# Performance work log

Measured on AMD Instinct MI355X. Metric: run time of the kernel, lower is better.

Reference implementation:

```python
import jax, jax.numpy as jnp
import numpy as np

N_HEAD = 16
N_EMBD = 2048


def _rope(x):
    # x: (B, H, L, D). FAITHFUL to source: _apply_rope unpacks (B, L, H, D) on a
    # (B, H, L, D) tensor, so rotation angle = head_index * inv_freq, broadcast over
    # all sequence positions (a latent bug in the original, reproduced exactly).
    B, H, L, D = x.shape
    inv_freq = 1.0 / (10000.0 ** (jnp.arange(0, D, 2, dtype=jnp.float32) / D))  # (D/2,)
    theta = jnp.arange(H, dtype=jnp.float32)[:, None] * inv_freq[None, :]       # (H, D/2)
    cos = jnp.cos(theta)[None, :, None, :]  # (1, H, 1, D/2)
    sin = jnp.sin(theta)[None, :, None, :]
    xp = x.astype(jnp.float32).reshape(B, H, L, D // 2, 2)
    x0, x1 = xp[..., 0], xp[..., 1]
    r0 = x0 * cos - x1 * sin
    r1 = x0 * sin + x1 * cos
    return jnp.stack([r0, r1], axis=-1).reshape(B, H, L, D).astype(x.dtype)


def setup_inputs() -> dict:
    key = jax.random.key(0)
    k1, k2, k3 = jax.random.split(key, 3)
    B, L, C = 2, 2048, N_EMBD
    s = 1.0 / np.sqrt(C).astype(np.float32)
    x = jax.random.normal(k1, (B, L, C), dtype=jnp.float32)
    w_attn = jax.random.normal(k2, (3 * C, C), dtype=jnp.float32) * s
    w_proj = jax.random.normal(k3, (C, C), dtype=jnp.float32) * s
    return {"x": x, "w_attn": w_attn, "w_proj": w_proj}


def reference(x, w_attn, w_proj):
    B, L, C = x.shape
    H = N_HEAD
    D = C // H
    qkv = x @ w_attn.T                       # (B, L, 3C)
    q, k, v = jnp.split(qkv, 3, axis=2)
    q = q.reshape(B, L, H, D).transpose(0, 2, 1, 3)  # (B, H, L, D)
    k = k.reshape(B, L, H, D).transpose(0, 2, 1, 3)
    v = v.reshape(B, L, H, D).transpose(0, 2, 1, 3)
    q = _rope(q)
    k = _rope(k)
    attn = jnp.einsum('bhqd,bhkd->bhqk', q, k) * (1.0 / np.sqrt(D).astype(np.float32))
    causal = jnp.tril(jnp.ones((L, L), dtype=bool))
    attn = jnp.where(causal[None, None], attn, -jnp.inf)
    attn = jax.nn.softmax(attn, axis=-1)
    y = jnp.einsum('bhqk,bhkd->bhqd', attn, v)
    y = y.transpose(0, 2, 1, 3).reshape(B, L, C)
    return y @ w_proj.T
```

## Files before the change

### kernel.cpp

```cpp
#include <hip/hip_runtime.h>

typedef __attribute__((ext_vector_type(8))) short bf16x8;
typedef __attribute__((ext_vector_type(4))) float f32x4;

__device__ __forceinline__ unsigned short f2bf(float f) {
  unsigned int u = __float_as_uint(f);
  u += 0x7FFF + ((u >> 16) & 1);
  return (unsigned short)(u >> 16);
}

__device__ __forceinline__ void gload_lds16(const void* g, void* l) {
  __builtin_amdgcn_global_load_lds(
      (const __attribute__((address_space(1))) unsigned int*)g,
      (__attribute__((address_space(3))) unsigned int*)l,
      16, 0, 0);
}

__global__ void cast_f32_to_bf16(const float* __restrict__ in,
                                 unsigned short* __restrict__ out, int n4) {
  int stride = gridDim.x * blockDim.x;
  for (int i = blockIdx.x * blockDim.x + threadIdx.x; i < n4; i += stride) {
    float4 v = ((const float4*)in)[i];
    ushort4 o;
    o.x = f2bf(v.x); o.y = f2bf(v.y); o.z = f2bf(v.z); o.w = f2bf(v.w);
    ((ushort4*)out)[i] = o;
  }
}

template<int EPI>
__global__ __launch_bounds__(256, 2)
void gemm_bt(const unsigned short* __restrict__ A,
             const unsigned short* __restrict__ Bw,
             float* __restrict__ Cf,
             unsigned short* __restrict__ Qo,
             unsigned short* __restrict__ Ko,
             unsigned short* __restrict__ Vo,
             int M, int N, int K, int Lseq) {
  __shared__ unsigned short As[128 * 32];
  __shared__ unsigned short Bs[128 * 32];
  const int tid = threadIdx.x;
  const int lane = tid & 63, w = tid >> 6;
  const int wm = w >> 1, wn = w & 1;
  const int g4 = lane >> 4, r16 = lane & 15;
  const long arow0 = (long)blockIdx.y * 128;
  const long brow0 = (long)blockIdx.x * 128;

  f32x4 acc[4][4];
#pragma unroll
  for (int i = 0; i < 4; ++i)
#pragma unroll
    for (int j = 0; j < 4; ++j) acc[i][j] = (f32x4){0.f, 0.f, 0.f, 0.f};

  for (int k0 = 0; k0 < K; k0 += 32) {
#pragma unroll
    for (int c = 0; c < 2; ++c) {
      int off = (w << 11) + (c << 10) + (lane << 4);
      int row = off >> 6;
      int cole = (off & 63) >> 1;
      gload_lds16(A + (arow0 + row) * (long)K + k0 + cole,
                  (char*)As + (w << 11) + (c << 10));
      gload_lds16(Bw + (brow0 + row) * (long)K + k0 + cole,
                  (char*)Bs + (w << 11) + (c << 10));
    }
    __syncthreads();
    bf16x8 af[4], bf[4];
#pragma unroll
    for (int mf = 0; mf < 4; ++mf)
      af[mf] = *(const bf16x8*)((const char*)As +
                                ((64 * wm + 16 * mf + r16) << 6) + (g4 << 4));
#pragma unroll
    for (int nf = 0; nf < 4; ++nf)
      bf[nf] = *(const bf16x8*)((const char*)Bs +
                                ((64 * wn + 16 * nf + r16) << 6) + (g4 << 4));
#pragma unroll
    for (int mf = 0; mf < 4; ++mf)
#pragma unroll
      for (int nf = 0; nf < 4; ++nf)
        acc[mf][nf] = __builtin_amdgcn_mfma_f32_16x16x32_bf16(
            af[mf], bf[nf], acc[mf][nf], 0, 0, 0);
    __syncthreads();
  }

  const float qscale = 0.08838834764831845f;
#pragma unroll
  for (int mf = 0; mf < 4; ++mf) {
#pragma unroll
    for (int nf = 0; nf < 4; ++nf) {
#pragma unroll
      for (int i = 0; i < 4; ++i) {
        long row = arow0 + 64 * wm + 16 * mf + 4 * g4 + i;
        long col = brow0 + 64 * wn + 16 * nf + r16;
        float v = acc[mf][nf][i];
        if (EPI == 0) {
          Cf[row * N + col] = v;
        } else {
          int which = (int)(col >> 11);
          int h = ((int)col >> 7) & 15;
          int d = (int)col & 127;
          int b = (int)(row >> 11);
          int l = (int)row & 2047;
          long bhead = (long)(b * 16 + h);
          if (which == 0)
            Qo[(bhead * Lseq + l) * 128 + d] = f2bf(v * qscale);
          else if (which == 1)
            Ko[(bhead * Lseq + l) * 128 + d] = f2bf(v);
          else
            Vo[(bhead * 128 + d) * Lseq + l] = f2bf(v);
        }
      }
    }
  }
}

__global__ __launch_bounds__(256, 2)
void attn_fwd(const unsigned short* __restrict__ Q,
              const unsigned short* __restrict__ K,
              const unsigned short* __restrict__ Vt,
              unsigned short* __restrict__ Y, int L) {
  const int D = 128;
  const int id = blockIdx.x;
  const int g = id & 7, kk = id >> 3;
  const int bh = (g << 2) + (kk >> 5);
  const int qt = 31 - (kk & 31);
  const int tid = threadIdx.x, lane = tid & 63, w = tid >> 6;
  const int g4 = lane >> 4, r16 = lane & 15;
  const int q0 = qt * 64;

  __shared__ unsigned short Klds[2 * 64 * 128];
  __shared__ unsigned short Vlds[2 * 128 * 64];
  __shared__ unsigned short P[4][16][72];

  const unsigned short* Qh = Q + (long)bh * L * D;
  const unsigned short* Kh = K + (long)bh * L * D;
  const unsigned short* Vh = Vt + (long)bh * D * L;

#define STAGE_TILE(kt_, buf_)                                                 \
  do {                                                                        \
    const int kbase_ = (kt_) * 64;                                            \
    _Pragma("unroll")                                                         \
    for (int r_ = 0; r_ < 4; ++r_) {                                          \
      int off_ = (tid << 4) + (r_ << 12);                                     \
      int krow_ = off_ >> 8, kcb_ = (off_ >> 4) & 15;                         \
      int kcbs_ = kcb_ ^ (krow_ & 7);                                         \
      gload_lds16(Kh + (long)(kbase_ + krow_) * 128 + kcbs_ * 8,              \
                  (char*)Klds + (buf_)*16384 + (w << 10) + (r_ << 12));       \
      int vrow_ = off_ >> 7, vcb_ = (off_ >> 4) & 7;                          \
      int vcbs_ = vcb_ ^ (vrow_ & 7);                                         \
      gload_lds16(Vh + (long)vrow_ * L + kbase_ + vcbs_ * 8,                  \
                  (char*)Vlds + (buf_)*16384 + (w << 10) + (r_ << 12));       \
    }                                                                         \
  } while (0)

  bf16x8 qf[4];
  {
    long qrow = q0 + 16 * w + r16;
#pragma unroll
    for (int ks = 0; ks < 4; ++ks)
      qf[ks] = *(const bf16x8*)(Qh + qrow * D + ks * 32 + g4 * 8);
  }
  f32x4 o[8];
#pragma unroll
  for (int j = 0; j < 8; ++j) o[j] = (f32x4){0.f, 0.f, 0.f, 0.f};
  float mrun[4] = {-1e30f, -1e30f, -1e30f, -1e30f};
  float lrun[4] = {0.f, 0.f, 0.f, 0.f};

  int cur = 0;
  STAGE_TILE(0, 0);

  for (int kt = 0; kt <= qt; ++kt) {
    if (kt < qt) {
      STAGE_TILE(kt + 1, cur ^ 1);
      asm volatile("s_waitcnt vmcnt(8)" ::: "memory");
    } else {
      asm volatile("s_waitcnt vmcnt(0)" ::: "memory");
    }
    __builtin_amdgcn_s_barrier();

    const char* Kl = (const char*)Klds + cur * 16384;
    const char* Vl = (const char*)Vlds + cur * 16384;

    f32x4 s[4];
#pragma unroll
    for (int nf = 0; nf < 4; ++nf) s[nf] = (f32x4){0.f, 0.f, 0.f, 0.f};
#pragma unroll
    for (int ks = 0; ks < 4; ++ks) {
#pragma unroll
      for (int nf = 0; nf < 4; ++nf) {
        int row = 16 * nf + r16;
        bf16x8 kf = *(const bf16x8*)(Kl + row * 256 +
                                     (((ks * 4 + g4) ^ (row & 7)) << 4));
        s[nf] = __builtin_amdgcn_mfma_f32_16x16x32_bf16(qf[ks], kf, s[nf], 0, 0, 0);
      }
    }

    const bool diag = (kt == qt);
#pragma unroll
    for (int i = 0; i < 4; ++i) {
      int qg = q0 + 16 * w + 4 * g4 + i;
      float sv[4];
      float rmax = -1e30f;
#pragma unroll
      for (int nf = 0; nf < 4; ++nf) {
        float t = s[nf][i];
        if (diag && (kt * 64 + 16 * nf + r16) > qg) t = -1e30f;
        sv[nf] = t;
        rmax = fmaxf(rmax, t);
      }
      rmax = fmaxf(rmax, __shfl_xor(rmax, 1));
      rmax = fmaxf(rmax, __shfl_xor(rmax, 2));
      rmax = fmaxf(rmax, __shfl_xor(rmax, 4));
      rmax = fmaxf(rmax, __shfl_xor(rmax, 8));
      float mnew = fmaxf(mrun[i], rmax);
      float corr = __expf(mrun[i] - mnew);
      mrun[i] = mnew;
      float rs = 0.f;
#pragma unroll
      for (int nf = 0; nf < 4; ++nf) {
        float pv = __expf(sv[nf] - mnew);
        P[w][4 * g4 + i][16 * nf + r16] = f2bf(pv);
        rs += pv;
      }
      rs += __shfl_xor(rs, 1);
      rs += __shfl_xor(rs, 2);
      rs += __shfl_xor(rs, 4);
      rs += __shfl_xor(rs, 8);
      lrun[i] = lrun[i] * corr + rs;
#pragma unroll
      for (int nf2 = 0; nf2 < 8; ++nf2) o[nf2][i] *= corr;
    }
#pragma unroll
    for (int ks2 = 0; ks2 < 2; ++ks2) {
      bf16x8 pf = *(const bf16x8*)(&P[w][r16][ks2 * 32 + g4 * 8]);
#pragma unroll
      for (int nf2 = 0; nf2 < 8; ++nf2) {
        int row = 16 * nf2 + r16;
        bf16x8 vf = *(const bf16x8*)(Vl + row * 128 +
                                     (((ks2 * 4 + g4) ^ (row & 7)) << 4));
        o[nf2] = __builtin_amdgcn_mfma_f32_16x16x32_bf16(pf, vf, o[nf2], 0, 0, 0);
      }
    }
    asm volatile("" ::: "memory");
    __builtin_amdgcn_s_barrier();
    cur ^= 1;
  }
#undef STAGE_TILE

  const int b = bh >> 4, h = bh & 15;
#pragma unroll
  for (int nf2 = 0; nf2 < 8; ++nf2) {
#pragma unroll
    for (int i = 0; i < 4; ++i) {
      long row = (long)b * L + q0 + 16 * w + 4 * g4 + i;
      float v = o[nf2][i] / lrun[i];
      Y[row * 2048 + h * 128 + 16 * nf2 + r16] = f2bf(v);
    }
  }
}

extern "C" void kernel_launch(void* const* d_in, const int* in_sizes, int n_in,
                              void* d_out, int out_size, void* d_ws,
                              size_t ws_size, hipStream_t stream) {
  const float* x = (const float*)d_in[0];
  const float* wa = (const float*)d_in[1];
  const float* wp = (const float*)d_in[2];
  float* out = (float*)d_out;
  const int B = 2, L = 2048, C = 2048;
  const int M = B * L;

  unsigned short* xb = (unsigned short*)d_ws;
  unsigned short* wab = xb + (size_t)M * C;
  unsigned short* wpb = wab + (size_t)3 * C * C;
  unsigned short* Qb = wpb + (size_t)C * C;
  unsigned short* Kb = Qb + (size_t)M * C;
  unsigned short* Vb = Kb + (size_t)M * C;
  unsigned short* Yb = Vb + (size_t)M * C;

  cast_f32_to_bf16<<<2048, 256, 0, stream>>>(x, xb, M * C / 4);
  cast_f32_to_bf16<<<2048, 256, 0, stream>>>(wa, wab, 3 * C * C / 4);
  cast_f32_to_bf16<<<1024, 256, 0, stream>>>(wp, wpb, C * C / 4);

  gemm_bt<1><<<dim3(3 * C / 128, M / 128), 256, 0, stream>>>(
      xb, wab, nullptr, Qb, Kb, Vb, M, 3 * C, C, L);

  attn_fwd<<<1024, 256, 0, stream>>>(Qb, Kb, Vb, Yb, L);

  gemm_bt<0><<<dim3(C / 128, M / 128), 256, 0, stream>>>(
      Yb, wpb, out, nullptr, nullptr, nullptr, M, C, C, L);
}
```

Before: 343.7 us.

## Double-buffer GEMM LDS tiles with swizzle, XCD-aware block remap, higher occupancy

The GEMM kernel now double-buffers its A/B LDS tiles and issues the next k-step's global-to-LDS loads before computing the current one, waiting with explicit vmcnt counters and raw barriers. This overlaps memory latency with MFMA work. It also XOR-swizzles the 16-byte column chunks to reduce LDS bank conflicts, and remaps the 1D block index across the 8 XCDs so that neighbouring tiles share L2. Launch bounds are raised to 4 waves per SIMD, which doubles LDS use per block and may add register pressure.

After: 345.7 us. About the same (+0.6%).

```diff
diff --git a/kernel.cpp b/kernel.cpp
--- a/kernel.cpp
+++ b/kernel.cpp
@@ -28,22 +28,40 @@
 }
 
 template<int EPI>
-__global__ __launch_bounds__(256, 2)
+__global__ __launch_bounds__(256, 4)
 void gemm_bt(const unsigned short* __restrict__ A,
              const unsigned short* __restrict__ Bw,
              float* __restrict__ Cf,
              unsigned short* __restrict__ Qo,
              unsigned short* __restrict__ Ko,
              unsigned short* __restrict__ Vo,
-             int M, int N, int K, int Lseq) {
-  __shared__ unsigned short As[128 * 32];
-  __shared__ unsigned short Bs[128 * 32];
+             int M, int N, int K, int Lseq, int nbx) {
+  __shared__ unsigned short As[2][128 * 32];
+  __shared__ unsigned short Bs[2][128 * 32];
   const int tid = threadIdx.x;
   const int lane = tid & 63, w = tid >> 6;
   const int wm = w >> 1, wn = w & 1;
   const int g4 = lane >> 4, r16 = lane & 15;
-  const long arow0 = (long)blockIdx.y * 128;
-  const long brow0 = (long)blockIdx.x * 128;
+
+  const int nwg = gridDim.x;
+  const int cpx = nwg >> 3;
+  const int bid = (blockIdx.x & 7) * cpx + (blockIdx.x >> 3);
+  const long arow0 = (long)(bid / nbx) * 128;
+  const long brow0 = (long)(bid % nbx) * 128;
+
+#define STAGE_G(k0_, buf_)                                                    \
+  do {                                                                        \
+    _Pragma("unroll")                                                         \
+    for (int c_ = 0; c_ < 2; ++c_) {                                          \
+      int off_ = (w << 11) + (c_ << 10) + (lane << 4);                        \
+      int row_ = off_ >> 6;                                                   \
+      int cbs_ = ((off_ >> 4) & 3) ^ ((row_ >> 1) & 3);                       \
+      gload_lds16(A + (arow0 + row_) * (long)K + (k0_) + cbs_ * 8,            \
+                  (char*)As[buf_] + off_);                                    \
+      gload_lds16(Bw + (brow0 + row_) * (long)K + (k0_) + cbs_ * 8,           \
+                  (char*)Bs[buf_] + off_);                                    \
+    }                                                                         \
+  } while (0)
 
   f32x4 acc[4][4];
 #pragma unroll
@@ -51,35 +69,40 @@
 #pragma unroll
     for (int j = 0; j < 4; ++j) acc[i][j] = (f32x4){0.f, 0.f, 0.f, 0.f};
 
-  for (int k0 = 0; k0 < K; k0 += 32) {
-#pragma unroll
-    for (int c = 0; c < 2; ++c) {
-      int off = (w << 11) + (c << 10) + (lane << 4);
-      int row = off >> 6;
-      int cole = (off & 63) >> 1;
-      gload_lds16(A + (arow0 + row) * (long)K + k0 + cole,
-                  (char*)As + (w << 11) + (c << 10));
-      gload_lds16(Bw + (brow0 + row) * (long)K + k0 + cole,
-                  (char*)Bs + (w << 11) + (c << 10));
-    }
-    __syncthreads();
+  const int T = K >> 5;
+  int cur = 0;
+  STAGE_G(0, 0);
+
+  for (int t = 0; t < T; ++t) {
+    if (t < T - 1) {
+      STAGE_G((t + 1) << 5, cur ^ 1);
+      asm volatile("s_waitcnt vmcnt(4)" ::: "memory");
+    } else {
+      asm volatile("s_waitcnt vmcnt(0)" ::: "memory");
+    }
+    __builtin_amdgcn_s_barrier();
+
+    const int rb = g4 ^ ((r16 >> 1) & 3);
     bf16x8 af[4], bf[4];
 #pragma unroll
     for (int mf = 0; mf < 4; ++mf)
-      af[mf] = *(const bf16x8*)((const char*)As +
-                                ((64 * wm + 16 * mf + r16) << 6) + (g4 << 4));
+      af[mf] = *(const bf16x8*)((const char*)As[cur] +
+                                ((64 * wm + 16 * mf + r16) << 6) + (rb << 4));
 #pragma unroll
     for (int nf = 0; nf < 4; ++nf)
-      bf[nf] = *(const bf16x8*)((const char*)Bs +
-                                ((64 * wn + 16 * nf + r16) << 6) + (g4 << 4));
+      bf[nf] = *(const bf16x8*)((const char*)Bs[cur] +
+                                ((64 * wn + 16 * nf + r16) << 6) + (rb << 4));
 #pragma unroll
     for (int mf = 0; mf < 4; ++mf)
 #pragma unroll
       for (int nf = 0; nf < 4; ++nf)
         acc[mf][nf] = __builtin_amdgcn_mfma_f32_16x16x32_bf16(
             af[mf], bf[nf], acc[mf][nf], 0, 0, 0);
-    __syncthreads();
-  }
+    asm volatile("" ::: "memory");
+    __builtin_amdgcn_s_barrier();
+    cur ^= 1;
+  }
+#undef STAGE_G
 
   const float qscale = 0.08838834764831845f;
 #pragma unroll
@@ -279,11 +302,11 @@
   cast_f32_to_bf16<<<2048, 256, 0, stream>>>(wa, wab, 3 * C * C / 4);
   cast_f32_to_bf16<<<1024, 256, 0, stream>>>(wp, wpb, C * C / 4);
 
-  gemm_bt<1><<<dim3(3 * C / 128, M / 128), 256, 0, stream>>>(
-      xb, wab, nullptr, Qb, Kb, Vb, M, 3 * C, C, L);
+  gemm_bt<1><<<(M / 128) * (3 * C / 128), 256, 0, stream>>>(
+      xb, wab, nullptr, Qb, Kb, Vb, M, 3 * C, C, L, 3 * C / 128);
 
   attn_fwd<<<1024, 256, 0, stream>>>(Qb, Kb, Vb, Yb, L);
 
-  gemm_bt<0><<<dim3(C / 128, M / 128), 256, 0, stream>>>(
-      Yb, wpb, out, nullptr, nullptr, nullptr, M, C, C, L);
-}
+  gemm_bt<0><<<(M / 128) * (C / 128), 256, 0, stream>>>(
+      Yb, wpb, out, nullptr, nullptr, nullptr, M, C, C, L, C / 128);
+}
```
